# Kernel tuning notes

Hardware: AMD Instinct MI355X
Metric: run time of the kernel (lower is better)

Reference implementation:

```python
import jax, jax.numpy as jnp
import numpy as np

D_HIDN = 64
SCALE = 1.0 / np.sqrt(D_HIDN).astype(np.float32)
MASK_FILL = -1e9


def setup_inputs() -> dict:
    key = jax.random.key(0)
    kq, kk, kv, km = jax.random.split(key, 4)
    B, H, S, D = 4, 16, 2048, 64
    Q = jax.random.normal(kq, (B, H, S, D), dtype=jnp.float32)
    K = jax.random.normal(kk, (B, H, S, D), dtype=jnp.float32)
    V = jax.random.normal(kv, (B, H, S, D), dtype=jnp.float32)
    attn_mask = jax.random.randint(km, (B, H, S, S), 0, 2).astype(jnp.bool_)
    return {"Q": Q, "K": K, "V": V, "attn_mask": attn_mask}


def reference(Q, K, V, attn_mask):
    # scores = Q K^T * scale  -> [B,H,S,S]
    scores = jnp.einsum("bhqd,bhkd->bhqk", Q, K) * SCALE
    scores = jnp.where(attn_mask, MASK_FILL, scores)
    attn_prob = jax.nn.softmax(scores, axis=-1)
    # dropout is identity in eval / deterministic reference
    context = jnp.einsum("bhqk,bhkd->bhqd", attn_prob, V)
    return (context, attn_prob)
```

## Files before the change

### kernel.cpp

```cpp
#include <hip/hip_runtime.h>
#include <stdint.h>

#define SEQ 2048
#define DIM 64
#define QBLK 16
#define NWAVE 8
#define KPW 256
#define NCT 16
#define NCHUNK 8
#define THREADS 512
#define SCALE 0.125f
#define LOG2E 1.4426950408889634f
#define PSTR 40
#define VPAD 18
#define NTSTR (32*VPAD + 8)

typedef __attribute__((ext_vector_type(4))) float f32x4;
typedef __attribute__((ext_vector_type(8))) __bf16 bf16x8;

static __device__ __forceinline__ unsigned bfbits(float x) {
    union { __bf16 b; unsigned short u; } cv; cv.b = (__bf16)x; return (unsigned)cv.u;
}
static __device__ __forceinline__ float lo16(unsigned u) { return __uint_as_float(u << 16); }
static __device__ __forceinline__ float hi16(unsigned u) { return __uint_as_float(u & 0xffff0000u); }

struct WaveBuf {
    union {
        __bf16 vbuf[4 * NTSTR];
        float  ctx[QBLK * DIM];
    };
};
struct SharedT {
    WaveBuf sw[NWAVE];
    __bf16 plds[NWAVE][QBLK][PSTR];
    float red_m[QBLK][NWAVE];
    float red_s[QBLK][NWAVE];
};

__global__ __launch_bounds__(THREADS, 4)
void sdpa_mfma7(const float* __restrict__ Q, const float* __restrict__ K,
                const float* __restrict__ V, const int* __restrict__ mask,
                float* __restrict__ ctx_out, float* __restrict__ prob_out) {
    __shared__ SharedT su;

    const int rb   = ((blockIdx.x & 7) << 10) + (blockIdx.x >> 3);
    const int bh   = rb >> 7;
    const int q0   = (rb & 127) * QBLK;
    const int t    = threadIdx.x;
    const int lane = t & 63;
    const int w    = t >> 6;
    const int g    = lane >> 4;
    const int c    = lane & 15;

    const size_t bh_off = (size_t)bh * SEQ * DIM;
    const float* Qb = Q + bh_off;
    const float* Kb = K + bh_off;
    const float* Vb = V + bh_off;
    const int*   Mb = mask + (size_t)bh * SEQ * SEQ;
    const int wbase = w * KPW;

    bf16x8 qf[2];
    {
        const float* qr = Qb + (size_t)(q0 + c) * DIM + 8 * g;
        #pragma unroll
        for (int h = 0; h < 2; ++h) {
            f32x4 a = *(const f32x4*)(qr + 32 * h);
            f32x4 b = *(const f32x4*)(qr + 32 * h + 4);
            bf16x8 f;
            f[0]=(__bf16)a[0]; f[1]=(__bf16)a[1]; f[2]=(__bf16)a[2]; f[3]=(__bf16)a[3];
            f[4]=(__bf16)b[0]; f[5]=(__bf16)b[1]; f[6]=(__bf16)b[2]; f[7]=(__bf16)b[3];
            qf[h] = f;
        }
    }

    unsigned sc_pk[2 * NCT];
    f32x4 kraw[2][4];
    int4  mraw[2];
    {
        const float* kr = Kb + (size_t)(wbase + c) * DIM + 8 * g;
        kraw[0][0] = *(const f32x4*)(kr);
        kraw[0][1] = *(const f32x4*)(kr + 4);
        kraw[0][2] = *(const f32x4*)(kr + 32);
        kraw[0][3] = *(const f32x4*)(kr + 36);
        mraw[0] = *(const int4*)(Mb + (size_t)(q0 + c) * SEQ + wbase + 4 * g);
    }
    #pragma unroll
    for (int ct = 0; ct < NCT; ++ct) {
        const int cur = ct & 1, nxt = cur ^ 1;
        if (ct + 1 < NCT) {
            const float* kr = Kb + (size_t)(wbase + (ct + 1) * 16 + c) * DIM + 8 * g;
            kraw[nxt][0] = *(const f32x4*)(kr);
            kraw[nxt][1] = *(const f32x4*)(kr + 4);
            kraw[nxt][2] = *(const f32x4*)(kr + 32);
            kraw[nxt][3] = *(const f32x4*)(kr + 36);
            mraw[nxt] = *(const int4*)(Mb + (size_t)(q0 + c) * SEQ + wbase + (ct + 1) * 16 + 4 * g);
        }
        bf16x8 kf0, kf1;
        {
            f32x4 a = kraw[cur][0], b = kraw[cur][1];
            kf0[0]=(__bf16)a[0]; kf0[1]=(__bf16)a[1]; kf0[2]=(__bf16)a[2]; kf0[3]=(__bf16)a[3];
            kf0[4]=(__bf16)b[0]; kf0[5]=(__bf16)b[1]; kf0[6]=(__bf16)b[2]; kf0[7]=(__bf16)b[3];
            a = kraw[cur][2]; b = kraw[cur][3];
            kf1[0]=(__bf16)a[0]; kf1[1]=(__bf16)a[1]; kf1[2]=(__bf16)a[2]; kf1[3]=(__bf16)a[3];
            kf1[4]=(__bf16)b[0]; kf1[5]=(__bf16)b[1]; kf1[6]=(__bf16)b[2]; kf1[7]=(__bf16)b[3];
        }
        f32x4 acc = {0.f, 0.f, 0.f, 0.f};
        acc = __builtin_amdgcn_mfma_f32_16x16x32_bf16(kf0, qf[0], acc, 0, 0, 0);
        acc = __builtin_amdgcn_mfma_f32_16x16x32_bf16(kf1, qf[1], acc, 0, 0, 0);
        int4 m = mraw[cur];
        float s0 = m.x ? -1e9f : acc[0] * SCALE;
        float s1 = m.y ? -1e9f : acc[1] * SCALE;
        float s2 = m.z ? -1e9f : acc[2] * SCALE;
        float s3 = m.w ? -1e9f : acc[3] * SCALE;
        sc_pk[2 * ct]     = bfbits(s0) | (bfbits(s1) << 16);
        sc_pk[2 * ct + 1] = bfbits(s2) | (bfbits(s3) << 16);
    }

    const int r_st = lane >> 4;
    const int cw   = (4 * c) & 15;
    const int ntw  = c >> 2;
    f32x4 vrawA[4], vrawB[4];
    {
        const float* vsrc = Vb + (size_t)(wbase + r_st) * DIM + 4 * c;
        #pragma unroll
        for (int i = 0; i < 4; ++i) {
            vrawA[i] = *(const f32x4*)(vsrc + (size_t)(4 * i) * DIM);
            vrawB[i] = *(const f32x4*)(vsrc + (size_t)(16 + 4 * i) * DIM);
        }
    }

    float mx = -3e38f;
    #pragma unroll
    for (int i = 0; i < 2 * NCT; ++i)
        mx = fmaxf(mx, fmaxf(lo16(sc_pk[i]), hi16(sc_pk[i])));
    mx = fmaxf(mx, __shfl_xor(mx, 16));
    mx = fmaxf(mx, __shfl_xor(mx, 32));
    if (g == 0) su.red_m[c][w] = mx;
    __syncthreads();
    float M = su.red_m[c][0];
    #pragma unroll
    for (int i = 1; i < NWAVE; ++i) M = fmaxf(M, su.red_m[c][i]);

    float sum = 0.f;
    #pragma unroll
    for (int i = 0; i < 2 * NCT; ++i) {
        float e0 = exp2f((lo16(sc_pk[i]) - M) * LOG2E);
        float e1 = exp2f((hi16(sc_pk[i]) - M) * LOG2E);
        sum += e0 + e1;
        sc_pk[i] = bfbits(e0) | (bfbits(e1) << 16);
    }
    sum += __shfl_xor(sum, 16);
    sum += __shfl_xor(sum, 32);
    if (g == 0) su.red_s[c][w] = sum;
    __syncthreads();
    float S = 0.f;
    #pragma unroll
    for (int i = 0; i < NWAVE; ++i) S += su.red_s[c][i];
    const float inv = 1.0f / S;
    float invr[4];
    #pragma unroll
    for (int jr = 0; jr < 4; ++jr) invr[jr] = __shfl(inv, 4 * g + jr);

    f32x4 cacc[4];
    #pragma unroll
    for (int nt = 0; nt < 4; ++nt) cacc[nt] = (f32x4){0.f, 0.f, 0.f, 0.f};

    float* prow = prob_out + ((size_t)bh * SEQ + (q0 + c)) * SEQ + wbase;
    __bf16* vbufW = su.sw[w].vbuf;

    #pragma unroll
    for (int cc = 0; cc < NCHUNK; ++cc) {
        #pragma unroll
        for (int i = 0; i < 4; ++i) {
            ushort2 lo_, hi_;
            lo_.x = (unsigned short)bfbits(vrawA[i][0]);
            lo_.y = (unsigned short)bfbits(vrawA[i][1]);
            hi_.x = (unsigned short)bfbits(vrawA[i][2]);
            hi_.y = (unsigned short)bfbits(vrawA[i][3]);
            __bf16* p = &vbufW[ntw * NTSTR + (4 * i + r_st) * VPAD + cw];
            *(ushort2*)p = lo_;
            *(ushort2*)(p + 2) = hi_;
        }
        #pragma unroll
        for (int i = 0; i < 4; ++i) {
            ushort2 lo_, hi_;
            lo_.x = (unsigned short)bfbits(vrawB[i][0]);
            lo_.y = (unsigned short)bfbits(vrawB[i][1]);
            hi_.x = (unsigned short)bfbits(vrawB[i][2]);
            hi_.y = (unsigned short)bfbits(vrawB[i][3]);
            __bf16* p = &vbufW[ntw * NTSTR + (16 + 4 * i + r_st) * VPAD + cw];
            *(ushort2*)p = lo_;
            *(ushort2*)(p + 2) = hi_;
        }

        if (cc + 1 < NCHUNK) {
            const float* vsrc = Vb + (size_t)(wbase + (cc + 1) * 32 + r_st) * DIM + 4 * c;
            #pragma unroll
            for (int i = 0; i < 4; ++i) {
                vrawA[i] = *(const f32x4*)(vsrc + (size_t)(4 * i) * DIM);
                vrawB[i] = *(const f32x4*)(vsrc + (size_t)(16 + 4 * i) * DIM);
            }
        }

        unsigned pkA0 = sc_pk[4 * cc], pkA1 = sc_pk[4 * cc + 1];
        unsigned pkB0 = sc_pk[4 * cc + 2], pkB1 = sc_pk[4 * cc + 3];
        {
            f32x4 pn0 = { lo16(pkA0) * inv, hi16(pkA0) * inv, lo16(pkA1) * inv, hi16(pkA1) * inv };
            f32x4 pn1 = { lo16(pkB0) * inv, hi16(pkB0) * inv, lo16(pkB1) * inv, hi16(pkB1) * inv };
            *(f32x4*)(prow + 32 * cc + 4 * g)      = pn0;
            *(f32x4*)(prow + 32 * cc + 16 + 4 * g) = pn1;
        }
        {
            uint2 ua; ua.x = pkA0; ua.y = pkA1;
            uint2 ub; ub.x = pkB0; ub.y = pkB1;
            *(uint2*)&su.plds[w][c][4 * g]      = ua;
            *(uint2*)&su.plds[w][c][16 + 4 * g] = ub;
        }
        bf16x8 pf = *(const bf16x8*)&su.plds[w][c][8 * g];

        bf16x8 vfr[4];
        #pragma unroll
        for (int nt = 0; nt < 4; ++nt) {
            bf16x8 f;
            #pragma unroll
            for (int j = 0; j < 8; ++j)
                f[j] = vbufW[nt * NTSTR + (8 * g + j) * VPAD + c];
            vfr[nt] = f;
        }

        __builtin_amdgcn_s_setprio(1);
        #pragma unroll
        for (int nt = 0; nt < 4; ++nt)
            cacc[nt] = __builtin_amdgcn_mfma_f32_16x16x32_bf16(pf, vfr[nt], cacc[nt], 0, 0, 0);
        __builtin_amdgcn_s_setprio(0);
    }

    #pragma unroll
    for (int nt = 0; nt < 4; ++nt)
        #pragma unroll
        for (int jr = 0; jr < 4; ++jr)
            su.sw[w].ctx[(4 * g + jr) * DIM + nt * 16 + c] = cacc[nt][jr] * invr[jr];
    __syncthreads();
    {
        int e = t * 2;
        float2 a = make_float2(0.f, 0.f);
        #pragma unroll
        for (int i = 0; i < NWAVE; ++i) {
            float2 v = *(const float2*)&su.sw[i].ctx[e];
            a.x += v.x; a.y += v.y;
        }
        *(float2*)(ctx_out + ((size_t)bh * SEQ + q0) * DIM + e) = a;
    }
}

extern "C" void kernel_launch(void* const* d_in, const int* in_sizes, int n_in,
                              void* d_out, int out_size, void* d_ws, size_t ws_size,
                              hipStream_t stream) {
    const float* Q = (const float*)d_in[0];
    const float* K = (const float*)d_in[1];
    const float* V = (const float*)d_in[2];
    const int* mask = (const int*)d_in[3];
    float* ctx  = (float*)d_out;
    float* prob = (float*)d_out + (size_t)4 * 16 * SEQ * DIM;

    dim3 grid(64 * (SEQ / QBLK));
    dim3 block(THREADS);
    sdpa_mfma7<<<grid, block, 0, stream>>>(Q, K, V, mask, ctx, prob);
}
```

Measured before the change: 1.060 ms.

## Use online softmax stats and recompute QK^T in second pass instead of storing scores

Each wave keeps only a running max and sum during the first QK^T pass. Mask bits are packed into two 32-bit registers, and the stored bf16 score array is dropped. The second pass recomputes QK^T with MFMA, re-reading K from global memory, to produce exact exponentials for the probability writes and the PV product. The mask is read with nontemporal loads and the probabilities are written with nontemporal stores. This trades the score-array registers and the double rounding of scores for extra MFMA work and a second read of K, which may cut register pressure but adds memory traffic and compute.

```diff
diff --git a/kernel.cpp b/kernel.cpp
--- a/kernel.cpp
+++ b/kernel.cpp
@@ -16,13 +16,18 @@
 #define NTSTR (32*VPAD + 8)
 
 typedef __attribute__((ext_vector_type(4))) float f32x4;
+typedef __attribute__((ext_vector_type(4))) int   i32x4;
 typedef __attribute__((ext_vector_type(8))) __bf16 bf16x8;
 
 static __device__ __forceinline__ unsigned bfbits(float x) {
     union { __bf16 b; unsigned short u; } cv; cv.b = (__bf16)x; return (unsigned)cv.u;
 }
-static __device__ __forceinline__ float lo16(unsigned u) { return __uint_as_float(u << 16); }
-static __device__ __forceinline__ float hi16(unsigned u) { return __uint_as_float(u & 0xffff0000u); }
+static __device__ __forceinline__ bf16x8 cvt8(f32x4 a, f32x4 b) {
+    bf16x8 f;
+    f[0]=(__bf16)a[0]; f[1]=(__bf16)a[1]; f[2]=(__bf16)a[2]; f[3]=(__bf16)a[3];
+    f[4]=(__bf16)b[0]; f[5]=(__bf16)b[1]; f[6]=(__bf16)b[2]; f[7]=(__bf16)b[3];
+    return f;
+}
 
 struct WaveBuf {
     union {
@@ -38,7 +43,7 @@
 };
 
 __global__ __launch_bounds__(THREADS, 4)
-void sdpa_mfma7(const float* __restrict__ Q, const float* __restrict__ K,
+void sdpa_mfma9(const float* __restrict__ Q, const float* __restrict__ K,
                 const float* __restrict__ V, const int* __restrict__ mask,
                 float* __restrict__ ctx_out, float* __restrict__ prob_out) {
     __shared__ SharedT su;
@@ -62,27 +67,21 @@
     bf16x8 qf[2];
     {
         const float* qr = Qb + (size_t)(q0 + c) * DIM + 8 * g;
-        #pragma unroll
-        for (int h = 0; h < 2; ++h) {
-            f32x4 a = *(const f32x4*)(qr + 32 * h);
-            f32x4 b = *(const f32x4*)(qr + 32 * h + 4);
-            bf16x8 f;
-            f[0]=(__bf16)a[0]; f[1]=(__bf16)a[1]; f[2]=(__bf16)a[2]; f[3]=(__bf16)a[3];
-            f[4]=(__bf16)b[0]; f[5]=(__bf16)b[1]; f[6]=(__bf16)b[2]; f[7]=(__bf16)b[3];
-            qf[h] = f;
-        }
-    }
-
-    unsigned sc_pk[2 * NCT];
+        qf[0] = cvt8(*(const f32x4*)(qr),      *(const f32x4*)(qr + 4));
+        qf[1] = cvt8(*(const f32x4*)(qr + 32), *(const f32x4*)(qr + 36));
+    }
+
+    float m_run = -1e30f, s_run = 0.f;
+    unsigned mbits0 = 0u, mbits1 = 0u;
     f32x4 kraw[2][4];
-    int4  mraw[2];
+    i32x4 mraw[2];
     {
         const float* kr = Kb + (size_t)(wbase + c) * DIM + 8 * g;
         kraw[0][0] = *(const f32x4*)(kr);
         kraw[0][1] = *(const f32x4*)(kr + 4);
         kraw[0][2] = *(const f32x4*)(kr + 32);
         kraw[0][3] = *(const f32x4*)(kr + 36);
-        mraw[0] = *(const int4*)(Mb + (size_t)(q0 + c) * SEQ + wbase + 4 * g);
+        mraw[0] = __builtin_nontemporal_load((const i32x4*)(Mb + (size_t)(q0 + c) * SEQ + wbase + 4 * g));
     }
     #pragma unroll
     for (int ct = 0; ct < NCT; ++ct) {
@@ -93,33 +92,36 @@
             kraw[nxt][1] = *(const f32x4*)(kr + 4);
             kraw[nxt][2] = *(const f32x4*)(kr + 32);
             kraw[nxt][3] = *(const f32x4*)(kr + 36);
-            mraw[nxt] = *(const int4*)(Mb + (size_t)(q0 + c) * SEQ + wbase + (ct + 1) * 16 + 4 * g);
-        }
-        bf16x8 kf0, kf1;
-        {
-            f32x4 a = kraw[cur][0], b = kraw[cur][1];
-            kf0[0]=(__bf16)a[0]; kf0[1]=(__bf16)a[1]; kf0[2]=(__bf16)a[2]; kf0[3]=(__bf16)a[3];
-            kf0[4]=(__bf16)b[0]; kf0[5]=(__bf16)b[1]; kf0[6]=(__bf16)b[2]; kf0[7]=(__bf16)b[3];
-            a = kraw[cur][2]; b = kraw[cur][3];
-            kf1[0]=(__bf16)a[0]; kf1[1]=(__bf16)a[1]; kf1[2]=(__bf16)a[2]; kf1[3]=(__bf16)a[3];
-            kf1[4]=(__bf16)b[0]; kf1[5]=(__bf16)b[1]; kf1[6]=(__bf16)b[2]; kf1[7]=(__bf16)b[3];
-        }
+            mraw[nxt] = __builtin_nontemporal_load(
+                (const i32x4*)(Mb + (size_t)(q0 + c) * SEQ + wbase + (ct + 1) * 16 + 4 * g));
+        }
+        bf16x8 kf0 = cvt8(kraw[cur][0], kraw[cur][1]);
+        bf16x8 kf1 = cvt8(kraw[cur][2], kraw[cur][3]);
         f32x4 acc = {0.f, 0.f, 0.f, 0.f};
         acc = __builtin_amdgcn_mfma_f32_16x16x32_bf16(kf0, qf[0], acc, 0, 0, 0);
         acc = __builtin_amdgcn_mfma_f32_16x16x32_bf16(kf1, qf[1], acc, 0, 0, 0);
-        int4 m = mraw[cur];
-        float s0 = m.x ? -1e9f : acc[0] * SCALE;
-        float s1 = m.y ? -1e9f : acc[1] * SCALE;
-        float s2 = m.z ? -1e9f : acc[2] * SCALE;
-        float s3 = m.w ? -1e9f : acc[3] * SCALE;
-        sc_pk[2 * ct]     = bfbits(s0) | (bfbits(s1) << 16);
-        sc_pk[2 * ct + 1] = bfbits(s2) | (bfbits(s3) << 16);
+        i32x4 mm = mraw[cur];
+        float x0 = mm[0] ? -1e9f : acc[0] * SCALE;
+        float x1 = mm[1] ? -1e9f : acc[1] * SCALE;
+        float x2 = mm[2] ? -1e9f : acc[2] * SCALE;
+        float x3 = mm[3] ? -1e9f : acc[3] * SCALE;
+        unsigned bp = (mm[0]?1u:0u) | (mm[1]?2u:0u) | (mm[2]?4u:0u) | (mm[3]?8u:0u);
+        if (ct < 8) mbits0 |= bp << (4 * ct); else mbits1 |= bp << (4 * (ct - 8));
+        float tmax = fmaxf(fmaxf(x0, x1), fmaxf(x2, x3));
+        float mnew = fmaxf(m_run, tmax);
+        float rs = exp2f((m_run - mnew) * LOG2E);
+        float e0 = exp2f((x0 - mnew) * LOG2E);
+        float e1 = exp2f((x1 - mnew) * LOG2E);
+        float e2 = exp2f((x2 - mnew) * LOG2E);
+        float e3 = exp2f((x3 - mnew) * LOG2E);
+        s_run = s_run * rs + ((e0 + e1) + (e2 + e3));
+        m_run = mnew;
     }
 
     const int r_st = lane >> 4;
     const int cw   = (4 * c) & 15;
     const int ntw  = c >> 2;
-    f32x4 vrawA[4], vrawB[4];
+    f32x4 vrawA[4], vrawB[4], krA[4], krB[4];
     {
         const float* vsrc = Vb + (size_t)(wbase + r_st) * DIM + 4 * c;
         #pragma unroll
@@ -127,39 +129,31 @@
             vrawA[i] = *(const f32x4*)(vsrc + (size_t)(4 * i) * DIM);
             vrawB[i] = *(const f32x4*)(vsrc + (size_t)(16 + 4 * i) * DIM);
         }
-    }
-
-    float mx = -3e38f;
-    #pragma unroll
-    for (int i = 0; i < 2 * NCT; ++i)
-        mx = fmaxf(mx, fmaxf(lo16(sc_pk[i]), hi16(sc_pk[i])));
-    mx = fmaxf(mx, __shfl_xor(mx, 16));
-    mx = fmaxf(mx, __shfl_xor(mx, 32));
-    if (g == 0) su.red_m[c][w] = mx;
+        const float* ka = Kb + (size_t)(wbase + c) * DIM + 8 * g;
+        krA[0] = *(const f32x4*)(ka);      krA[1] = *(const f32x4*)(ka + 4);
+        krA[2] = *(const f32x4*)(ka + 32); krA[3] = *(const f32x4*)(ka + 36);
+        const float* kb = Kb + (size_t)(wbase + 16 + c) * DIM + 8 * g;
+        krB[0] = *(const f32x4*)(kb);      krB[1] = *(const f32x4*)(kb + 4);
+        krB[2] = *(const f32x4*)(kb + 32); krB[3] = *(const f32x4*)(kb + 36);
+    }
+
+    float mw = fmaxf(m_run, __shfl_xor(m_run, 16));
+    mw = fmaxf(mw, __shfl_xor(mw, 32));
+    if (g == 0) su.red_m[c][w] = mw;
     __syncthreads();
     float M = su.red_m[c][0];
     #pragma unroll
     for (int i = 1; i < NWAVE; ++i) M = fmaxf(M, su.red_m[c][i]);
 
-    float sum = 0.f;
-    #pragma unroll
-    for (int i = 0; i < 2 * NCT; ++i) {
-        float e0 = exp2f((lo16(sc_pk[i]) - M) * LOG2E);
-        float e1 = exp2f((hi16(sc_pk[i]) - M) * LOG2E);
-        sum += e0 + e1;
-        sc_pk[i] = bfbits(e0) | (bfbits(e1) << 16);
-    }
-    sum += __shfl_xor(sum, 16);
-    sum += __shfl_xor(sum, 32);
-    if (g == 0) su.red_s[c][w] = sum;
+    float sadj = s_run * exp2f((m_run - M) * LOG2E);
+    sadj += __shfl_xor(sadj, 16);
+    sadj += __shfl_xor(sadj, 32);
+    if (g == 0) su.red_s[c][w] = sadj;
     __syncthreads();
     float S = 0.f;
     #pragma unroll
     for (int i = 0; i < NWAVE; ++i) S += su.red_s[c][i];
     const float inv = 1.0f / S;
-    float invr[4];
-    #pragma unroll
-    for (int jr = 0; jr < 4; ++jr) invr[jr] = __shfl(inv, 4 * g + jr);
 
     f32x4 cacc[4];
     #pragma unroll
@@ -192,7 +186,6 @@
             *(ushort2*)p = lo_;
             *(ushort2*)(p + 2) = hi_;
         }
-
         if (cc + 1 < NCHUNK) {
             const float* vsrc = Vb + (size_t)(wbase + (cc + 1) * 32 + r_st) * DIM + 4 * c;
             #pragma unroll
@@ -202,17 +195,63 @@
             }
         }
 
-        unsigned pkA0 = sc_pk[4 * cc], pkA1 = sc_pk[4 * cc + 1];
-        unsigned pkB0 = sc_pk[4 * cc + 2], pkB1 = sc_pk[4 * cc + 3];
+        f32x4 eA, eB;
         {
-            f32x4 pn0 = { lo16(pkA0) * inv, hi16(pkA0) * inv, lo16(pkA1) * inv, hi16(pkA1) * inv };
-            f32x4 pn1 = { lo16(pkB0) * inv, hi16(pkB0) * inv, lo16(pkB1) * inv, hi16(pkB1) * inv };
-            *(f32x4*)(prow + 32 * cc + 4 * g)      = pn0;
-            *(f32x4*)(prow + 32 * cc + 16 + 4 * g) = pn1;
+            bf16x8 kf0 = cvt8(krA[0], krA[1]);
+            bf16x8 kf1 = cvt8(krA[2], krA[3]);
+            f32x4 acc = {0.f, 0.f, 0.f, 0.f};
+            acc = __builtin_amdgcn_mfma_f32_16x16x32_bf16(kf0, qf[0], acc, 0, 0, 0);
+            acc = __builtin_amdgcn_mfma_f32_16x16x32_bf16(kf1, qf[1], acc, 0, 0, 0);
+            if (cc + 1 < NCHUNK) {
+                const float* ka = Kb + (size_t)(wbase + (2 * cc + 2) * 16 + c) * DIM + 8 * g;
+                krA[0] = *(const f32x4*)(ka);      krA[1] = *(const f32x4*)(ka + 4);
+                krA[2] = *(const f32x4*)(ka + 32); krA[3] = *(const f32x4*)(ka + 36);
+            }
+            unsigned bq = ((cc < 4) ? (mbits0 >> (8 * cc)) : (mbits1 >> (8 * (cc - 4)))) & 0xFu;
+            float x0 = (bq & 1u) ? -1e9f : acc[0] * SCALE;
+            float x1 = (bq & 2u) ? -1e9f : acc[1] * SCALE;
+            float x2 = (bq & 4u) ? -1e9f : acc[2] * SCALE;
+            float x3 = (bq & 8u) ? -1e9f : acc[3] * SCALE;
+            eA[0] = exp2f((x0 - M) * LOG2E);
+            eA[1] = exp2f((x1 - M) * LOG2E);
+            eA[2] = exp2f((x2 - M) * LOG2E);
+            eA[3] = exp2f((x3 - M) * LOG2E);
         }
         {
-            uint2 ua; ua.x = pkA0; ua.y = pkA1;
-            uint2 ub; ub.x = pkB0; ub.y = pkB1;
+            bf16x8 kf0 = cvt8(krB[0], krB[1]);
+            bf16x8 kf1 = cvt8(krB[2], krB[3]);
+            f32x4 acc = {0.f, 0.f, 0.f, 0.f};
+            acc = __builtin_amdgcn_mfma_f32_16x16x32_bf16(kf0, qf[0], acc, 0, 0, 0);
+            acc = __builtin_amdgcn_mfma_f32_16x16x32_bf16(kf1, qf[1], acc, 0, 0, 0);
+            if (cc + 1 < NCHUNK) {
+                const float* kb = Kb + (size_t)(wbase + (2 * cc + 3) * 16 + c) * DIM + 8 * g;
+                krB[0] = *(const f32x4*)(kb);      krB[1] = *(const f32x4*)(kb + 4);
+                krB[2] = *(const f32x4*)(kb + 32); krB[3] = *(const f32x4*)(kb + 36);
+            }
+            unsigned bq = ((cc < 4) ? (mbits0 >> (8 * cc + 4)) : (mbits1 >> (8 * (cc - 4) + 4))) & 0xFu;
+            float x0 = (bq & 1u) ? -1e9f : acc[0] * SCALE;
+            float x1 = (bq & 2u) ? -1e9f : acc[1] * SCALE;
+            float x2 = (bq & 4u) ? -1e9f : acc[2] * SCALE;
+            float x3 = (bq & 8u) ? -1e9f : acc[3] * SCALE;
+            eB[0] = exp2f((x0 - M) * LOG2E);
+            eB[1] = exp2f((x1 - M) * LOG2E);
+            eB[2] = exp2f((x2 - M) * LOG2E);
+            eB[3] = exp2f((x3 - M) * LOG2E);
+        }
+
+        {
+            f32x4 pnA = { eA[0] * inv, eA[1] * inv, eA[2] * inv, eA[3] * inv };
+            f32x4 pnB = { eB[0] * inv, eB[1] * inv, eB[2] * inv, eB[3] * inv };
+            __builtin_nontemporal_store(pnA, (f32x4*)(prow + 32 * cc + 4 * g));
+            __builtin_nontemporal_store(pnB, (f32x4*)(prow + 32 * cc + 16 + 4 * g));
+        }
+
+        {
+            uint2 ua, ub;
+            ua.x = bfbits(eA[0]) | (bfbits(eA[1]) << 16);
+            ua.y = bfbits(eA[2]) | (bfbits(eA[3]) << 16);
+            ub.x = bfbits(eB[0]) | (bfbits(eB[1]) << 16);
+            ub.y = bfbits(eB[2]) | (bfbits(eB[3]) << 16);
             *(uint2*)&su.plds[w][c][4 * g]      = ua;
             *(uint2*)&su.plds[w][c][16 + 4 * g] = ub;
         }
@@ -235,6 +274,9 @@
         __builtin_amdgcn_s_setprio(0);
     }
 
+    float invr[4];
+    #pragma unroll
+    for (int jr = 0; jr < 4; ++jr) invr[jr] = __shfl(inv, 4 * g + jr);
     #pragma unroll
     for (int nt = 0; nt < 4; ++nt)
         #pragma unroll
@@ -265,5 +307,5 @@
 
     dim3 grid(64 * (SEQ / QBLK));
     dim3 block(THREADS);
-    sdpa_mfma7<<<grid, block, 0, stream>>>(Q, K, V, mask, ctx, prob);
+    sdpa_mfma9<<<grid, block, 0, stream>>>(Q, K, V, mask, ctx, prob);
 }
```

Result: slower. 2.222 ms (+109.7%).
